# Kernel tuning notes

Measured on AMD Instinct MI355X. Metric: run time of the kernel, lower is better.

The kernel has to match this reference:

```python
import jax, jax.numpy as jnp
import numpy as np

KERNEL = 7
STRIDE = 3
C_IN, C_OUT = 3, 4
HIDDEN, OUTPUT = 64, 10
H_OUT = (32 - KERNEL) // STRIDE + 1  # 9
FC1_IN = C_OUT * H_OUT * H_OUT       # 324


def setup_inputs() -> dict:
    key = jax.random.key(0)
    ks = jax.random.split(key, 6)
    B = 16384
    x = jax.random.normal(ks[0], (B, C_IN, 32, 32), dtype=jnp.float32)
    conv_w = jax.random.normal(ks[1], (C_OUT, C_IN, KERNEL, KERNEL), dtype=jnp.float32) * 0.05
    fc1_w = jax.random.normal(ks[2], (HIDDEN, FC1_IN), dtype=jnp.float32) * (1.0 / np.sqrt(FC1_IN))
    fc1_b = jax.random.normal(ks[3], (HIDDEN,), dtype=jnp.float32) * 0.01
    fc2_w = jax.random.normal(ks[4], (OUTPUT, HIDDEN), dtype=jnp.float32) * (1.0 / np.sqrt(HIDDEN))
    fc2_b = jax.random.normal(ks[5], (OUTPUT,), dtype=jnp.float32) * 0.01
    return {"x": x, "conv_w": conv_w, "fc1_w": fc1_w, "fc1_b": fc1_b, "fc2_w": fc2_w, "fc2_b": fc2_b}


def reference(x, conv_w, fc1_w, fc1_b, fc2_w, fc2_b):
    # conv (NO bias, matching original forward which only uses conv1.weight)
    y = jax.lax.conv_general_dilated(
        x, conv_w, window_strides=(STRIDE, STRIDE), padding='VALID',
        dimension_numbers=('NCHW', 'OIHW', 'NCHW'))  # [B, 4, 9, 9]
    y = y * y
    y = y.reshape(y.shape[0], -1)                    # [B, 324]
    h = y @ fc1_w.T + fc1_b                          # [B, 64]
    h = h * h
    out = h @ fc2_w.T + fc2_b                        # [B, 10]
    return out
```

## Files before the change

kernel.cpp:

```cpp
#include <hip/hip_runtime.h>
#include <string.h>


typedef _Float16 f16;
typedef f16 f16x8 __attribute__((ext_vector_type(8)));
typedef __fp16 fp16x2 __attribute__((ext_vector_type(2)));
typedef float f32x4 __attribute__((ext_vector_type(4)));

#define YS_B   27648
#define LDS_B  (27648 + 11520)

__device__ __forceinline__ unsigned pack_rtz(float a, float b) {
    fp16x2 h = __builtin_amdgcn_cvt_pkrtz(a, b);
    unsigned u; memcpy(&u, &h, 4); return u;
}

__device__ __forceinline__ void write_windows(f16* wptr, const float4 ldv[8]) {
    unsigned h[16];
#pragma unroll
    for (int i = 0; i < 8; ++i) {
        h[2*i]   = pack_rtz(ldv[i].x, ldv[i].y);
        h[2*i+1] = pack_rtz(ldv[i].z, ldv[i].w);
    }
#pragma unroll
    for (int ow = 0; ow < 9; ow += 2) {
        int d = (3 * ow) >> 1;
        uint4 v; v.x = h[d]; v.y = h[d+1]; v.z = h[d+2]; v.w = h[d+3];
        *reinterpret_cast<uint4*>(wptr + ow * 8) = v;
    }
#pragma unroll
    for (int ow = 1; ow < 9; ow += 2) {
        int d = (3 * ow) >> 1;
        uint4 v;
        v.x = __builtin_amdgcn_alignbit(h[d+1], h[d],   16);
        v.y = __builtin_amdgcn_alignbit(h[d+2], h[d+1], 16);
        v.z = __builtin_amdgcn_alignbit(h[d+3], h[d+2], 16);
        v.w = __builtin_amdgcn_alignbit(h[d+4], h[d+3], 16);
        *reinterpret_cast<uint4*>(wptr + ow * 8) = v;
    }
}

__device__ __forceinline__ void split_hi_lo(float4 v0, float4 v1, f16x8& bh, f16x8& bl) {
    float v[8] = {v0.x, v0.y, v0.z, v0.w, v1.x, v1.y, v1.z, v1.w};
#pragma unroll
    for (int j = 0; j < 8; ++j) {
        f16 hi = (f16)v[j];
        bh[j] = hi;
        bl[j] = (f16)(v[j] - (float)hi);
    }
}

__global__ __launch_bounds__(256, 4) void convnet_mfma(
    const float* __restrict__ x,
    const float* __restrict__ cw,
    const float* __restrict__ fc1w,
    const float* __restrict__ fc1b,
    const float* __restrict__ fc2w,
    const float* __restrict__ fc2b,
    float* __restrict__ out)
{
    __shared__ unsigned char lds[LDS_B];
    f16* WINH = (f16*)lds;
    f16* YS   = (f16*)(lds + YS_B);
    float* HSQ = (float*)lds;

    const int t    = threadIdx.x;
    const int lane = t & 63;
    const int w    = t >> 6;
    const int g    = lane >> 4;
    const int lr   = lane & 15;
    const size_t base_s = (size_t)blockIdx.x * 16;

    f16x8 wcf[6];
#pragma unroll
    for (int st = 0; st < 6; ++st) {
        f16x8 v = {0, 0, 0, 0, 0, 0, 0, 0};
        int seg = st * 4 + g;
        if (lr < 4 && seg <= 20) {
            int ci = seg >= 14 ? 2 : (seg >= 7 ? 1 : 0);
            int kh = seg - ci * 7;
            const float* wr = cw + ((lr * 3 + ci) * 7 + kh) * 7;
#pragma unroll
            for (int j = 0; j < 7; ++j) v[j] = (f16)wr[j];
        }
        wcf[st] = v;
    }

    int seg2off[6];
#pragma unroll
    for (int st = 0; st < 6; ++st) {
        int seg  = st * 4 + g;
        int segc = seg > 20 ? 20 : seg;
        int ci   = segc >= 14 ? 2 : (segc >= 7 ? 1 : 0);
        int kh   = segc - ci * 7;
        seg2off[st] = ci * 4608 + kh * 144;
    }
    const int u = 3 - w;
    const int ntiles = (u == 3) ? 2 : 3;
    int rowbase[3], coff[3][4];
#pragma unroll
    for (int ti = 0; ti < 3; ++ti) {
        int tile = u + ti * 4;
        int tc   = tile > 10 ? 10 : tile;
        int grow = tc * 16 + lr;
        int growc = grow > 161 ? 161 : grow;
        int sp  = growc >= 81;
        int p   = growc - (sp ? 81 : 0);
        int oh  = (p * 57) >> 9;
        int ow  = p - oh * 9;
        rowbase[ti] = sp * 13824 + oh * 432 + ow * 16;
#pragma unroll
        for (int r = 0; r < 4; ++r) {
            int gr = tc * 16 + g * 4 + r;
            if (ti < ntiles && gr < 162) {
                int sp2 = gr >= 81;
                int p2  = gr - (sp2 ? 81 : 0);
                coff[ti][r] = sp2 * 360 + lr * 81 + p2;
            } else coff[ti][r] = -1;
        }
    }

    const bool stg = t < 192;
    const int ssp  = (t >= 96) ? 1 : 0;
    const int srem = t - ssp * 96;
    const int sci  = srem >> 5;
    const int srow = srem & 31;
    const int goff = sci * 1024 + srow * 32;
    f16* wptr = WINH + ssp * 6912 + sci * 2304 + srow * 72;

    float4 ldv[8];
    if (stg) {
        const float* gp = x + (base_s + ssp) * 3072 + goff;
#pragma unroll
        for (int i = 0; i < 8; ++i) ldv[i] = *(const float4*)(gp + 4 * i);
    }
#pragma unroll
    for (int i = 0; i < 3; ++i) {
        int idx = i * 256 + t;
        if (idx < 720) *(f32x4*)(lds + YS_B + idx * 16) = f32x4{0.f, 0.f, 0.f, 0.f};
    }
    if (stg) write_windows(wptr, ldv);
    __syncthreads();

    for (int pair = 0; pair < 8; ++pair) {
        if (pair < 7 && stg) {
            const float* gp = x + (base_s + (size_t)(pair + 1) * 2 + ssp) * 3072 + goff;
#pragma unroll
            for (int i = 0; i < 8; ++i) ldv[i] = *(const float4*)(gp + 4 * i);
        }
        f16* ysp = YS + pair * 720;
        __builtin_amdgcn_s_setprio(1);
#pragma unroll
        for (int ti = 0; ti < 3; ++ti) {
            if (ti < ntiles) {
                const unsigned char* pA = lds + rowbase[ti];
                f32x4 acc = {0.f, 0.f, 0.f, 0.f};
#pragma unroll
                for (int st = 0; st < 6; ++st) {
                    f16x8 af = *(const f16x8*)(pA + seg2off[st]);
                    acc = __builtin_amdgcn_mfma_f32_16x16x32_f16(af, wcf[st], acc, 0, 0, 0);
                }
                if (lr < 4) {
#pragma unroll
                    for (int r = 0; r < 4; ++r) {
                        int off = coff[ti][r];
                        if (off >= 0) {
                            float y = acc[r];
                            ysp[off] = (f16)(y * y);
                        }
                    }
                }
            }
        }
        __builtin_amdgcn_s_setprio(0);
        __syncthreads();
        if (pair < 7) {
            if (stg) write_windows(wptr, ldv);
            __syncthreads();
        }
    }

    {
        f32x4 a1 = {0.f, 0.f, 0.f, 0.f};
        const int n = w * 16 + lr;
        const float* w1r = fc1w + n * 324;
        __builtin_amdgcn_s_setprio(1);
#pragma unroll
        for (int st = 0; st < 10; ++st) {
            f16x8 av = *(const f16x8*)(YS + lr * 360 + st * 32 + g * 8);
            float4 v0 = *(const float4*)(w1r + st * 32 + g * 8);
            float4 v1 = *(const float4*)(w1r + st * 32 + g * 8 + 4);
            f16x8 bh, bl;
            split_hi_lo(v0, v1, bh, bl);
            a1 = __builtin_amdgcn_mfma_f32_16x16x32_f16(av, bh, a1, 0, 0, 0);
            a1 = __builtin_amdgcn_mfma_f32_16x16x32_f16(av, bl, a1, 0, 0, 0);
        }
        {
            f16x8 av = *(const f16x8*)(YS + lr * 360 + 320 + g * 8);
            f16x8 bh = {0,0,0,0,0,0,0,0}, bl = {0,0,0,0,0,0,0,0};
            if (g == 0) {
                float4 v0 = *(const float4*)(w1r + 320);
                float v[4] = {v0.x, v0.y, v0.z, v0.w};
#pragma unroll
                for (int j = 0; j < 4; ++j) {
                    f16 hi = (f16)v[j];
                    bh[j] = hi;
                    bl[j] = (f16)(v[j] - (float)hi);
                }
            }
            a1 = __builtin_amdgcn_mfma_f32_16x16x32_f16(av, bh, a1, 0, 0, 0);
            a1 = __builtin_amdgcn_mfma_f32_16x16x32_f16(av, bl, a1, 0, 0, 0);
        }
        __builtin_amdgcn_s_setprio(0);
        float bias = fc1b[n];
#pragma unroll
        for (int r = 0; r < 4; ++r) {
            int s = g * 4 + r;
            float h = a1[r] + bias;
            HSQ[s * 65 + n] = h * h;
        }
    }
    __syncthreads();

    if (t < 160) {
        int sj = t / 10, j = t - sj * 10;
        float a = fc2b[j];
        const float* wr = fc2w + j * 64;
        const float* hv = &HSQ[sj * 65];
#pragma unroll
        for (int i = 0; i < 64; ++i) a += wr[i] * hv[i];
        out[(base_s + sj) * 10 + j] = a;
    }
}

extern "C" void kernel_launch(void* const* d_in, const int* in_sizes, int n_in,
                              void* d_out, int out_size, void* d_ws, size_t ws_size,
                              hipStream_t stream) {
    const float* x    = (const float*)d_in[0];
    const float* cw   = (const float*)d_in[1];
    const float* fc1w = (const float*)d_in[2];
    const float* fc1b = (const float*)d_in[3];
    const float* fc2w = (const float*)d_in[4];
    const float* fc2b = (const float*)d_in[5];
    float* out = (float*)d_out;

    const int B = in_sizes[0] / 3072;
    hipLaunchKernelGGL(convnet_mfma, dim3(B / 16), dim3(256), 0, stream,
                       x, cw, fc1w, fc1b, fc2w, fc2b, out);
}
```

Measured before the change: 46.43 us.

## Stage one sample per iteration to halve window LDS and raise occupancy

The conv stage now stages one sample per iteration instead of two, with each staging thread loading half a row (5 float4) and writing half of the im2col windows. This halves the window LDS buffer and cuts per-thread load registers, and launch bounds rise from 4 to 6 blocks per CU to get more resident waves. In exchange there are twice as many loop iterations and barriers per block, fewer MFMA tiles per iteration, and some overlap between the two halves' loads.

```diff
diff --git a/kernel.cpp b/kernel.cpp
--- a/kernel.cpp
+++ b/kernel.cpp
@@ -7,50 +7,53 @@
 typedef __fp16 fp16x2 __attribute__((ext_vector_type(2)));
 typedef float f32x4 __attribute__((ext_vector_type(4)));
 
-#define YS_B   27648
-#define LDS_B  (27648 + 11520)
+#define YS_B   13824
+#define LDS_B  (13824 + 11520)
 
 __device__ __forceinline__ unsigned pack_rtz(float a, float b) {
     fp16x2 h = __builtin_amdgcn_cvt_pkrtz(a, b);
     unsigned u; memcpy(&u, &h, 4); return u;
 }
 
-__device__ __forceinline__ void write_windows(f16* wptr, const float4 ldv[8]) {
-    unsigned h[16];
-#pragma unroll
-    for (int i = 0; i < 8; ++i) {
+__device__ __forceinline__ void write_half(f16* wptr, const float4 ldv[5], int half) {
+    unsigned h[10];
+#pragma unroll
+    for (int i = 0; i < 5; ++i) {
         h[2*i]   = pack_rtz(ldv[i].x, ldv[i].y);
         h[2*i+1] = pack_rtz(ldv[i].z, ldv[i].w);
     }
-#pragma unroll
-    for (int ow = 0; ow < 9; ow += 2) {
-        int d = (3 * ow) >> 1;
-        uint4 v; v.x = h[d]; v.y = h[d+1]; v.z = h[d+2]; v.w = h[d+3];
-        *reinterpret_cast<uint4*>(wptr + ow * 8) = v;
-    }
-#pragma unroll
-    for (int ow = 1; ow < 9; ow += 2) {
-        int d = (3 * ow) >> 1;
+    const int owb = half * 4;
+    if (!half) {
+        uint4 v; v.x = h[0]; v.y = h[1]; v.z = h[2]; v.w = h[3];
+        *reinterpret_cast<uint4*>(wptr) = v;
+    }
+    {
         uint4 v;
-        v.x = __builtin_amdgcn_alignbit(h[d+1], h[d],   16);
-        v.y = __builtin_amdgcn_alignbit(h[d+2], h[d+1], 16);
-        v.z = __builtin_amdgcn_alignbit(h[d+3], h[d+2], 16);
-        v.w = __builtin_amdgcn_alignbit(h[d+4], h[d+3], 16);
-        *reinterpret_cast<uint4*>(wptr + ow * 8) = v;
-    }
-}
-
-__device__ __forceinline__ void split_hi_lo(float4 v0, float4 v1, f16x8& bh, f16x8& bl) {
-    float v[8] = {v0.x, v0.y, v0.z, v0.w, v1.x, v1.y, v1.z, v1.w};
-#pragma unroll
-    for (int j = 0; j < 8; ++j) {
-        f16 hi = (f16)v[j];
-        bh[j] = hi;
-        bl[j] = (f16)(v[j] - (float)hi);
-    }
-}
-
-__global__ __launch_bounds__(256, 4) void convnet_mfma(
+        v.x = __builtin_amdgcn_alignbit(h[2], h[1], 16);
+        v.y = __builtin_amdgcn_alignbit(h[3], h[2], 16);
+        v.z = __builtin_amdgcn_alignbit(h[4], h[3], 16);
+        v.w = __builtin_amdgcn_alignbit(h[5], h[4], 16);
+        *reinterpret_cast<uint4*>(wptr + (owb + 1) * 8) = v;
+    }
+    {
+        uint4 v; v.x = h[3]; v.y = h[4]; v.z = h[5]; v.w = h[6];
+        *reinterpret_cast<uint4*>(wptr + (owb + 2) * 8) = v;
+    }
+    {
+        uint4 v;
+        v.x = __builtin_amdgcn_alignbit(h[5], h[4], 16);
+        v.y = __builtin_amdgcn_alignbit(h[6], h[5], 16);
+        v.z = __builtin_amdgcn_alignbit(h[7], h[6], 16);
+        v.w = __builtin_amdgcn_alignbit(h[8], h[7], 16);
+        *reinterpret_cast<uint4*>(wptr + (owb + 3) * 8) = v;
+    }
+    {
+        uint4 v; v.x = h[6]; v.y = h[7]; v.z = h[8]; v.w = h[9];
+        *reinterpret_cast<uint4*>(wptr + (owb + 4) * 8) = v;
+    }
+}
+
+__global__ __launch_bounds__(256, 6) void convnet_mfma(
     const float* __restrict__ x,
     const float* __restrict__ cw,
     const float* __restrict__ fc1w,
@@ -95,63 +98,54 @@
         int kh   = segc - ci * 7;
         seg2off[st] = ci * 4608 + kh * 144;
     }
+
     const int u = 3 - w;
-    const int ntiles = (u == 3) ? 2 : 3;
-    int rowbase[3], coff[3][4];
-#pragma unroll
-    for (int ti = 0; ti < 3; ++ti) {
+    const int ntiles = (u < 2) ? 2 : 1;
+    int rowbase[2], pbase[2];
+#pragma unroll
+    for (int ti = 0; ti < 2; ++ti) {
         int tile = u + ti * 4;
-        int tc   = tile > 10 ? 10 : tile;
+        int tc   = tile > 5 ? 5 : tile;
         int grow = tc * 16 + lr;
-        int growc = grow > 161 ? 161 : grow;
-        int sp  = growc >= 81;
-        int p   = growc - (sp ? 81 : 0);
-        int oh  = (p * 57) >> 9;
-        int ow  = p - oh * 9;
-        rowbase[ti] = sp * 13824 + oh * 432 + ow * 16;
-#pragma unroll
-        for (int r = 0; r < 4; ++r) {
-            int gr = tc * 16 + g * 4 + r;
-            if (ti < ntiles && gr < 162) {
-                int sp2 = gr >= 81;
-                int p2  = gr - (sp2 ? 81 : 0);
-                coff[ti][r] = sp2 * 360 + lr * 81 + p2;
-            } else coff[ti][r] = -1;
-        }
-    }
-
-    const bool stg = t < 192;
-    const int ssp  = (t >= 96) ? 1 : 0;
-    const int srem = t - ssp * 96;
-    const int sci  = srem >> 5;
-    const int srow = srem & 31;
-    const int goff = sci * 1024 + srow * 32;
-    f16* wptr = WINH + ssp * 6912 + sci * 2304 + srow * 72;
-
-    float4 ldv[8];
+        int p    = grow > 80 ? 80 : grow;
+        int oh   = (p * 57) >> 9;
+        int ow   = p - oh * 9;
+        rowbase[ti] = oh * 432 + ow * 16;
+        pbase[ti]   = tc * 16 + g * 4;
+    }
+
+    const bool stg  = t < 192;
+    const int  r_   = t >> 1;
+    const int  half = t & 1;
+    const int  sci  = r_ >> 5;
+    const int  srow = r_ & 31;
+    const int  goff = sci * 1024 + srow * 32 + (half ? 12 : 0);
+    f16* wptr = WINH + sci * 2304 + srow * 72;
+
+    float4 ldv[5];
     if (stg) {
-        const float* gp = x + (base_s + ssp) * 3072 + goff;
-#pragma unroll
-        for (int i = 0; i < 8; ++i) ldv[i] = *(const float4*)(gp + 4 * i);
+        const float* gp = x + base_s * 3072 + goff;
+#pragma unroll
+        for (int i = 0; i < 5; ++i) ldv[i] = *(const float4*)(gp + 4 * i);
     }
 #pragma unroll
     for (int i = 0; i < 3; ++i) {
         int idx = i * 256 + t;
         if (idx < 720) *(f32x4*)(lds + YS_B + idx * 16) = f32x4{0.f, 0.f, 0.f, 0.f};
     }
-    if (stg) write_windows(wptr, ldv);
+    if (stg) write_half(wptr, ldv, half);
     __syncthreads();
 
-    for (int pair = 0; pair < 8; ++pair) {
-        if (pair < 7 && stg) {
-            const float* gp = x + (base_s + (size_t)(pair + 1) * 2 + ssp) * 3072 + goff;
-#pragma unroll
-            for (int i = 0; i < 8; ++i) ldv[i] = *(const float4*)(gp + 4 * i);
-        }
-        f16* ysp = YS + pair * 720;
+    for (int s = 0; s < 16; ++s) {
+        if (s < 15 && stg) {
+            const float* gp = x + (base_s + s + 1) * 3072 + goff;
+#pragma unroll
+            for (int i = 0; i < 5; ++i) ldv[i] = *(const float4*)(gp + 4 * i);
+        }
+        f16* ysp = YS + s * 360;
         __builtin_amdgcn_s_setprio(1);
 #pragma unroll
-        for (int ti = 0; ti < 3; ++ti) {
+        for (int ti = 0; ti < 2; ++ti) {
             if (ti < ntiles) {
                 const unsigned char* pA = lds + rowbase[ti];
                 f32x4 acc = {0.f, 0.f, 0.f, 0.f};
@@ -163,10 +157,10 @@
                 if (lr < 4) {
 #pragma unroll
                     for (int r = 0; r < 4; ++r) {
-                        int off = coff[ti][r];
-                        if (off >= 0) {
+                        int p = pbase[ti] + r;
+                        if (p < 81) {
                             float y = acc[r];
-                            ysp[off] = (f16)(y * y);
+                            ysp[lr * 81 + p] = (f16)(y * y);
                         }
                     }
                 }
@@ -174,8 +168,8 @@
         }
         __builtin_amdgcn_s_setprio(0);
         __syncthreads();
-        if (pair < 7) {
-            if (stg) write_windows(wptr, ldv);
+        if (s < 15) {
+            if (stg) write_half(wptr, ldv, half);
             __syncthreads();
         }
     }
@@ -190,8 +184,14 @@
             f16x8 av = *(const f16x8*)(YS + lr * 360 + st * 32 + g * 8);
             float4 v0 = *(const float4*)(w1r + st * 32 + g * 8);
             float4 v1 = *(const float4*)(w1r + st * 32 + g * 8 + 4);
+            float vv[8] = {v0.x, v0.y, v0.z, v0.w, v1.x, v1.y, v1.z, v1.w};
             f16x8 bh, bl;
-            split_hi_lo(v0, v1, bh, bl);
+#pragma unroll
+            for (int j = 0; j < 8; ++j) {
+                f16 hi = (f16)vv[j];
+                bh[j] = hi;
+                bl[j] = (f16)(vv[j] - (float)hi);
+            }
             a1 = __builtin_amdgcn_mfma_f32_16x16x32_f16(av, bh, a1, 0, 0, 0);
             a1 = __builtin_amdgcn_mfma_f32_16x16x32_f16(av, bl, a1, 0, 0, 0);
         }
@@ -200,12 +200,12 @@
             f16x8 bh = {0,0,0,0,0,0,0,0}, bl = {0,0,0,0,0,0,0,0};
             if (g == 0) {
                 float4 v0 = *(const float4*)(w1r + 320);
-                float v[4] = {v0.x, v0.y, v0.z, v0.w};
+                float vv[4] = {v0.x, v0.y, v0.z, v0.w};
 #pragma unroll
                 for (int j = 0; j < 4; ++j) {
-                    f16 hi = (f16)v[j];
+                    f16 hi = (f16)vv[j];
                     bh[j] = hi;
-                    bl[j] = (f16)(v[j] - (float)hi);
+                    bl[j] = (f16)(vv[j] - (float)hi);
                 }
             }
             a1 = __builtin_amdgcn_mfma_f32_16x16x32_f16(av, bh, a1, 0, 0, 0);
```

New measurement: 45.50 us. -2.0%, faster.
